# Kernel optimization log

Hardware: AMD Instinct MI355X
Metric: run time of the kernel (lower is better)

Reference implementation:

```python
import jax, jax.numpy as jnp
import numpy as np

QWEN_H = 2048
SNN_H = 512


def setup_inputs() -> dict:
    key = jax.random.key(0)
    k0, k1, k2, k3, k4 = jax.random.split(key, 5)
    hidden_states = jax.random.normal(k0, (4, 2048, QWEN_H), dtype=jnp.float32)
    # nn.Linear weights stored as [out, in]
    w_down = jax.random.normal(k1, (SNN_H, QWEN_H), dtype=jnp.float32) / np.sqrt(QWEN_H)
    w_up = jax.random.normal(k2, (QWEN_H, SNN_H), dtype=jnp.float32) / np.sqrt(SNN_H)
    w1 = jax.random.normal(k3, (SNN_H, SNN_H), dtype=jnp.float32) / np.sqrt(SNN_H)
    w2 = jax.random.normal(k4, (SNN_H, SNN_H), dtype=jnp.float32) / np.sqrt(SNN_H)
    residual_scale = jnp.float32(0.1)
    return {"hidden_states": hidden_states, "w_down": w_down, "w_up": w_up,
            "w1": w1, "w2": w2, "residual_scale": residual_scale}


def reference(hidden_states, w_down, w_up, w1, w2, residual_scale):
    # Faithful math of SNNMiddleLayer.forward. The spike pulse encode ->
    # SpikeFP32Linear (fp32 accumulation) -> pulse decode path is a lossless
    # FP32 spike encoding of an ordinary bias-free linear layer, so the
    # per-timestep loop computes exactly out_t = w2 @ (w1 @ proj_down(x_t)),
    # which we express as fused batched GEMMs over all timesteps.
    residual = hidden_states
    x = jnp.einsum('bsq,hq->bsh', hidden_states, w_down)   # proj_down
    h = jnp.einsum('bsh,oh->bso', x, w1)                   # snn_linear1
    o = jnp.einsum('bso,po->bsp', h, w2)                   # snn_linear2
    out = jnp.einsum('bsp,qp->bsq', o, w_up)               # proj_up
    return residual + residual_scale * out
```

## Files before the change

### kernel.cpp

```cpp
#include <hip/hip_runtime.h>
#include <hip/hip_bf16.h>
#include <stdint.h>

using bf16 = __hip_bfloat16;
typedef __attribute__((ext_vector_type(8))) short bf16x8;
typedef __attribute__((ext_vector_type(4))) float f32x4;

__device__ __forceinline__ void async_load16(const void* g, void* l) {
    __builtin_amdgcn_global_load_lds(
        (__attribute__((address_space(1))) const void*)g,
        (__attribute__((address_space(3))) void*)l,
        16, 0, 0);
}

__device__ __forceinline__ void cvt_block_2048(const float* __restrict__ src,
                                               bf16* __restrict__ dst, int relblk) {
    int i = (relblk * 256 + (int)threadIdx.x) * 8;
    float4 f0 = *(const float4*)(src + i);
    float4 f1 = *(const float4*)(src + i + 4);
    union { bf16 h[8]; uint4 u; } o;
    o.h[0] = __float2bfloat16(f0.x); o.h[1] = __float2bfloat16(f0.y);
    o.h[2] = __float2bfloat16(f0.z); o.h[3] = __float2bfloat16(f0.w);
    o.h[4] = __float2bfloat16(f1.x); o.h[5] = __float2bfloat16(f1.y);
    o.h[6] = __float2bfloat16(f1.z); o.h[7] = __float2bfloat16(f1.w);
    *(uint4*)(dst + i) = o.u;
}

__device__ __forceinline__ void transp_tile(const float* __restrict__ src,
                                            bf16* __restrict__ dst, int R, int C,
                                            int tile, int ntx, bf16 (*sh)[33]) {
    const int bx = (tile % ntx) * 32, by = (tile / ntx) * 32;
    const int lx = threadIdx.x & 31;
    const int ly4 = ((int)threadIdx.x >> 5) * 4;
#pragma unroll
    for (int r = 0; r < 4; ++r)
        sh[ly4 + r][lx] = __float2bfloat16(src[(size_t)(by + ly4 + r) * C + bx + lx]);
    __syncthreads();
#pragma unroll
    for (int r = 0; r < 4; ++r)
        dst[(size_t)(bx + ly4 + r) * R + by + lx] = sh[lx][ly4 + r];
}

__global__ __launch_bounds__(256) void prep(
    const float* __restrict__ hs, bf16* __restrict__ hsb,
    const float* __restrict__ w1, bf16* __restrict__ w1b,
    const float* __restrict__ wup, bf16* __restrict__ wub,
    const float* __restrict__ wd, bf16* __restrict__ wdt,
    const float* __restrict__ w2, bf16* __restrict__ w2t) {
    __shared__ bf16 sh[32][33];
    int b = blockIdx.x;
    if (b < 8192)       cvt_block_2048(hs, hsb, b);
    else if (b < 8320)  cvt_block_2048(w1, w1b, b - 8192);
    else if (b < 8832)  cvt_block_2048(wup, wub, b - 8320);
    else if (b < 9856)  transp_tile(wd, wdt, 512, 2048, b - 8832, 64, sh);
    else                transp_tile(w2, w2t, 512, 512, b - 9856, 16, sh);
}

template<int BN, int EPI>
__device__ __forceinline__ void gemm_core(
    const bf16* __restrict__ A, const bf16* __restrict__ B,
    bf16* __restrict__ Cb, float* __restrict__ Cf,
    const float* __restrict__ Res, const float* __restrict__ sp,
    int N, int K, int bxi, int byi, bf16* As, bf16* Bs)
{
    constexpr int BM = 128;
    constexpr int NJ = BN / 32;
    static_assert(BN == 64 || BN == 128, "BN");

    const int tid  = threadIdx.x;
    const int wave = tid >> 6;
    const int lane = tid & 63;
    const int wm = wave >> 1, wn = wave & 1;
    const size_t bm = (size_t)bxi * BM;
    const size_t bn = (size_t)byi * BN;

    f32x4 acc[4][NJ];
#pragma unroll
    for (int i = 0; i < 4; ++i)
#pragma unroll
        for (int j = 0; j < NJ; ++j)
            acc[i][j] = (f32x4){0.f, 0.f, 0.f, 0.f};

    const int srow  = lane >> 3;
    const int scol8 = (lane & 7) ^ srow;

    for (int k0 = 0; k0 < K; k0 += 64) {
        constexpr int TOT = (BM + BN) / 8;
#pragma unroll
        for (int c = 0; c < TOT / 4; ++c) {
            const int cc = wave + c * 4;
            if (cc < BM / 8) {
                const int rb = cc * 8;
                async_load16(A + (bm + rb + srow) * (size_t)K + k0 + scol8 * 8, &As[rb * 64]);
            } else {
                const int rb = (cc - BM / 8) * 8;
                async_load16(B + (bn + rb + srow) * (size_t)K + k0 + scol8 * 8, &Bs[rb * 64]);
            }
        }
        __syncthreads();

#pragma unroll
        for (int kk = 0; kk < 2; ++kk) {
            bf16x8 af[4], bfr[NJ];
#pragma unroll
            for (int i = 0; i < 4; ++i) {
                const int r  = wm * 64 + i * 16 + (lane & 15);
                const int c8 = kk * 4 + (lane >> 4);
                af[i] = *(const bf16x8*)&As[(size_t)(r * 8 + (c8 ^ (r & 7))) * 8];
            }
#pragma unroll
            for (int j = 0; j < NJ; ++j) {
                const int r  = wn * (BN / 2) + j * 16 + (lane & 15);
                const int c8 = kk * 4 + (lane >> 4);
                bfr[j] = *(const bf16x8*)&Bs[(size_t)(r * 8 + (c8 ^ (r & 7))) * 8];
            }
#pragma unroll
            for (int i = 0; i < 4; ++i)
#pragma unroll
                for (int j = 0; j < NJ; ++j)
                    acc[i][j] = __builtin_amdgcn_mfma_f32_16x16x32_bf16(af[i], bfr[j], acc[i][j], 0, 0, 0);
        }
        __syncthreads();
    }

    const int col_l = lane & 15;
    const int row_l = (lane >> 4) * 4;
    if (EPI == 0) {
#pragma unroll
        for (int i = 0; i < 4; ++i)
#pragma unroll
            for (int j = 0; j < NJ; ++j)
#pragma unroll
                for (int r = 0; r < 4; ++r) {
                    size_t row = bm + wm * 64 + i * 16 + row_l + r;
                    size_t col = bn + wn * (BN / 2) + j * 16 + col_l;
                    Cb[row * (size_t)N + col] = __float2bfloat16(acc[i][j][r]);
                }
    } else {
        const float s = *sp;
        float* lds_f = (float*)As + wave * (16 * 68);
#pragma unroll
        for (int i = 0; i < 4; ++i) {
#pragma unroll
            for (int j = 0; j < NJ; ++j)
#pragma unroll
                for (int r = 0; r < 4; ++r)
                    lds_f[(row_l + r) * 68 + j * 16 + col_l] = acc[i][j][r];
            __syncthreads();
#pragma unroll
            for (int rh = 0; rh < 2; ++rh)
#pragma unroll
                for (int ch = 0; ch < 2; ++ch) {
                    const int r16 = rh * 8 + (lane >> 3);
                    const int cb  = (lane & 7) * 4 + ch * 32;
                    float4 v = *(float4*)&lds_f[r16 * 68 + cb];
                    size_t row = bm + wm * 64 + i * 16 + r16;
                    size_t col = bn + wn * 64 + cb;
                    size_t idx = row * (size_t)N + col;
                    float4 rv = *(const float4*)&Res[idx];
                    float4 o;
                    o.x = rv.x + s * v.x; o.y = rv.y + s * v.y;
                    o.z = rv.z + s * v.z; o.w = rv.w + s * v.w;
                    *(float4*)&Cf[idx] = o;
                }
            __syncthreads();
        }
    }
}

template<int BN, int EPI>
__global__ __launch_bounds__(256) void gemm_bf16(
    const bf16* __restrict__ A, const bf16* __restrict__ B,
    bf16* __restrict__ Cb, float* __restrict__ Cf,
    const float* __restrict__ Res, const float* __restrict__ sp, int N, int K) {
    __shared__ __align__(16) bf16 smem[(128 + BN) * 64];
    gemm_core<BN, EPI>(A, B, Cb, Cf, Res, sp, N, K, blockIdx.y, blockIdx.x,
                       smem, smem + 128 * 64);
}

__global__ __launch_bounds__(256) void gemm_ru(
    const bf16* __restrict__ A0, const bf16* __restrict__ B0, bf16* __restrict__ C0,
    int N0, int K0, int nb0, int nt0,
    const bf16* __restrict__ A1, const bf16* __restrict__ B1, bf16* __restrict__ C1,
    int N1, int K1, int nt1) {
    __shared__ __align__(16) bf16 smem[(128 + 64) * 64];
    int b = blockIdx.x;
    if (b < nb0)
        gemm_core<64, 0>(A0, B0, C0, nullptr, nullptr, nullptr, N0, K0,
                         b / nt0, b % nt0, smem, smem + 128 * 64);
    else {
        b -= nb0;
        gemm_core<64, 0>(A1, B1, C1, nullptr, nullptr, nullptr, N1, K1,
                         b / nt1, b % nt1, smem, smem + 128 * 64);
    }
}

extern "C" void kernel_launch(void* const* d_in, const int* in_sizes, int n_in,
                              void* d_out, int out_size, void* d_ws, size_t ws_size,
                              hipStream_t stream) {
    const float* hs     = (const float*)d_in[0];
    const float* w_down = (const float*)d_in[1];
    const float* w_up   = (const float*)d_in[2];
    const float* w1     = (const float*)d_in[3];
    const float* w2     = (const float*)d_in[4];
    const float* rs     = (const float*)d_in[5];

    char* ws = (char*)d_ws;
    bf16* hs_b  = (bf16*)(ws + 0);
    bf16* x_b   = (bf16*)(ws + 33554432);
    bf16* w1_b  = (bf16*)(ws + 41943040);
    bf16* wu_b  = (bf16*)(ws + 42467328);
    bf16* wdt_b = (bf16*)(ws + 44564480);
    bf16* w2t_b = (bf16*)(ws + 46661632);
    bf16* Rm    = (bf16*)(ws + 47185920);
    bf16* Um    = (bf16*)(ws + 49283072);

    prep<<<dim3(10112), dim3(256), 0, stream>>>(hs, hs_b, w1, w1_b, w_up, wu_b,
                                                w_down, wdt_b, w2, w2t_b);
    gemm_ru<<<dim3(256), dim3(256), 0, stream>>>(w1_b, wdt_b, Rm, 2048, 512, 128, 32,
                                                 wu_b, w2t_b, Um, 512, 512, 8);
    gemm_bf16<64, 0><<<dim3(8, 64), dim3(256), 0, stream>>>(hs_b, Rm, x_b, nullptr,
                                                            nullptr, nullptr, 512, 2048);
    gemm_bf16<128, 1><<<dim3(16, 64), dim3(256), 0, stream>>>(x_b, Um, nullptr, (float*)d_out,
                                                              hs, rs, 2048, 512);
}
```

Before: 218.5 us.

## Overlap hidden-state conversion with weight GEMMs, double K-step, prefetch residual

Moves the large fp32-to-bf16 conversion of hidden_states out of the weight-prep kernel into the same launch as the small weight-product GEMMs. The bulk conversion then fills the GPU alongside those few blocks instead of serialising before them. The big down-projection GEMM now stages two 64-wide K slices per barrier, halving the number of synchronisations at the cost of doubled LDS. The final GEMM loads half of its residual tile into registers before the main loop so that global read overlaps the MFMA work, which raises register pressure.

```diff
diff --git a/kernel.cpp b/kernel.cpp
--- a/kernel.cpp
+++ b/kernel.cpp
@@ -26,37 +26,31 @@
     *(uint4*)(dst + i) = o.u;
 }
 
-__device__ __forceinline__ void transp_tile(const float* __restrict__ src,
-                                            bf16* __restrict__ dst, int R, int C,
-                                            int tile, int ntx, bf16 (*sh)[33]) {
-    const int bx = (tile % ntx) * 32, by = (tile / ntx) * 32;
-    const int lx = threadIdx.x & 31;
-    const int ly4 = ((int)threadIdx.x >> 5) * 4;
-#pragma unroll
-    for (int r = 0; r < 4; ++r)
-        sh[ly4 + r][lx] = __float2bfloat16(src[(size_t)(by + ly4 + r) * C + bx + lx]);
-    __syncthreads();
-#pragma unroll
-    for (int r = 0; r < 4; ++r)
-        dst[(size_t)(bx + ly4 + r) * R + by + lx] = sh[lx][ly4 + r];
-}
-
-__global__ __launch_bounds__(256) void prep(
-    const float* __restrict__ hs, bf16* __restrict__ hsb,
+__global__ __launch_bounds__(256) void prep_w(
     const float* __restrict__ w1, bf16* __restrict__ w1b,
     const float* __restrict__ wup, bf16* __restrict__ wub,
     const float* __restrict__ wd, bf16* __restrict__ wdt,
     const float* __restrict__ w2, bf16* __restrict__ w2t) {
     __shared__ bf16 sh[32][33];
     int b = blockIdx.x;
-    if (b < 8192)       cvt_block_2048(hs, hsb, b);
-    else if (b < 8320)  cvt_block_2048(w1, w1b, b - 8192);
-    else if (b < 8832)  cvt_block_2048(wup, wub, b - 8320);
-    else if (b < 9856)  transp_tile(wd, wdt, 512, 2048, b - 8832, 64, sh);
-    else                transp_tile(w2, w2t, 512, 512, b - 9856, 16, sh);
-}
-
-template<int BN, int EPI>
+    if (b < 128)       { cvt_block_2048(w1, w1b, b); return; }
+    if (b < 640)       { cvt_block_2048(wup, wub, b - 128); return; }
+    const float* src; bf16* dst; int R, C, tile, ntx;
+    if (b < 1664) { src = wd; dst = wdt; R = 512; C = 2048; tile = b - 640; ntx = 64; }
+    else          { src = w2; dst = w2t; R = 512; C = 512;  tile = b - 1664; ntx = 16; }
+    const int bx = (tile % ntx) * 32, by = (tile / ntx) * 32;
+    const int lx = threadIdx.x & 31;
+    const int ly4 = ((int)threadIdx.x >> 5) * 4;
+#pragma unroll
+    for (int r = 0; r < 4; ++r)
+        sh[ly4 + r][lx] = __float2bfloat16(src[(size_t)(by + ly4 + r) * C + bx + lx]);
+    __syncthreads();
+#pragma unroll
+    for (int r = 0; r < 4; ++r)
+        dst[(size_t)(bx + ly4 + r) * R + by + lx] = sh[lx][ly4 + r];
+}
+
+template<int BN, int EPI, int NP>
 __device__ __forceinline__ void gemm_core(
     const bf16* __restrict__ A, const bf16* __restrict__ B,
     bf16* __restrict__ Cb, float* __restrict__ Cf,
@@ -84,35 +78,56 @@
     const int srow  = lane >> 3;
     const int scol8 = (lane & 7) ^ srow;
 
-    for (int k0 = 0; k0 < K; k0 += 64) {
+    float4 res_pre[EPI ? 8 : 1];
+    if (EPI) {
+        const int r16 = lane >> 3;
+        const int cbb = (lane & 7) * 4;
+#pragma unroll
+        for (int i = 0; i < 2; ++i)
+#pragma unroll
+            for (int rh = 0; rh < 2; ++rh)
+#pragma unroll
+                for (int ch = 0; ch < 2; ++ch) {
+                    size_t row = bm + wm * 64 + i * 16 + rh * 8 + r16;
+                    size_t col = bn + wn * 64 + cbb + ch * 32;
+                    res_pre[i * 4 + rh * 2 + ch] = *(const float4*)&Res[row * (size_t)N + col];
+                }
+    }
+
+    for (int k0 = 0; k0 < K; k0 += 64 * NP) {
         constexpr int TOT = (BM + BN) / 8;
 #pragma unroll
-        for (int c = 0; c < TOT / 4; ++c) {
-            const int cc = wave + c * 4;
-            if (cc < BM / 8) {
-                const int rb = cc * 8;
-                async_load16(A + (bm + rb + srow) * (size_t)K + k0 + scol8 * 8, &As[rb * 64]);
-            } else {
-                const int rb = (cc - BM / 8) * 8;
-                async_load16(B + (bn + rb + srow) * (size_t)K + k0 + scol8 * 8, &Bs[rb * 64]);
+        for (int p = 0; p < NP; ++p)
+#pragma unroll
+            for (int c = 0; c < TOT / 4; ++c) {
+                const int cc = wave + c * 4;
+                if (cc < BM / 8) {
+                    const int rb = cc * 8;
+                    async_load16(A + (bm + rb + srow) * (size_t)K + k0 + p * 64 + scol8 * 8,
+                                 &As[p * BM * 64 + rb * 64]);
+                } else {
+                    const int rb = (cc - BM / 8) * 8;
+                    async_load16(B + (bn + rb + srow) * (size_t)K + k0 + p * 64 + scol8 * 8,
+                                 &Bs[p * BN * 64 + rb * 64]);
+                }
             }
-        }
         __syncthreads();
 
 #pragma unroll
-        for (int kk = 0; kk < 2; ++kk) {
+        for (int kk = 0; kk < 2 * NP; ++kk) {
+            const bf16* Ap = As + (kk >> 1) * BM * 64;
+            const bf16* Bp = Bs + (kk >> 1) * BN * 64;
+            const int c8 = (kk & 1) * 4 + (lane >> 4);
             bf16x8 af[4], bfr[NJ];
 #pragma unroll
             for (int i = 0; i < 4; ++i) {
-                const int r  = wm * 64 + i * 16 + (lane & 15);
-                const int c8 = kk * 4 + (lane >> 4);
-                af[i] = *(const bf16x8*)&As[(size_t)(r * 8 + (c8 ^ (r & 7))) * 8];
+                const int r = wm * 64 + i * 16 + (lane & 15);
+                af[i] = *(const bf16x8*)&Ap[(size_t)(r * 8 + (c8 ^ (r & 7))) * 8];
             }
 #pragma unroll
             for (int j = 0; j < NJ; ++j) {
-                const int r  = wn * (BN / 2) + j * 16 + (lane & 15);
-                const int c8 = kk * 4 + (lane >> 4);
-                bfr[j] = *(const bf16x8*)&Bs[(size_t)(r * 8 + (c8 ^ (r & 7))) * 8];
+                const int r = wn * (BN / 2) + j * 16 + (lane & 15);
+                bfr[j] = *(const bf16x8*)&Bp[(size_t)(r * 8 + (c8 ^ (r & 7))) * 8];
             }
 #pragma unroll
             for (int i = 0; i < 4; ++i)
@@ -157,7 +172,8 @@
                     size_t row = bm + wm * 64 + i * 16 + r16;
                     size_t col = bn + wn * 64 + cb;
                     size_t idx = row * (size_t)N + col;
-                    float4 rv = *(const float4*)&Res[idx];
+                    float4 rv = (i < 2) ? res_pre[i * 4 + rh * 2 + ch]
+                                        : *(const float4*)&Res[idx];
                     float4 o;
                     o.x = rv.x + s * v.x; o.y = rv.y + s * v.y;
                     o.z = rv.z + s * v.z; o.w = rv.w + s * v.w;
@@ -168,31 +184,31 @@
     }
 }
 
-template<int BN, int EPI>
+template<int BN, int EPI, int NP>
 __global__ __launch_bounds__(256) void gemm_bf16(
     const bf16* __restrict__ A, const bf16* __restrict__ B,
     bf16* __restrict__ Cb, float* __restrict__ Cf,
     const float* __restrict__ Res, const float* __restrict__ sp, int N, int K) {
-    __shared__ __align__(16) bf16 smem[(128 + BN) * 64];
-    gemm_core<BN, EPI>(A, B, Cb, Cf, Res, sp, N, K, blockIdx.y, blockIdx.x,
-                       smem, smem + 128 * 64);
-}
-
-__global__ __launch_bounds__(256) void gemm_ru(
+    __shared__ __align__(16) bf16 smem[(128 + BN) * 64 * NP];
+    gemm_core<BN, EPI, NP>(A, B, Cb, Cf, Res, sp, N, K, blockIdx.y, blockIdx.x,
+                           smem, smem + 128 * 64 * NP);
+}
+
+__global__ __launch_bounds__(256) void ru_cvt(
     const bf16* __restrict__ A0, const bf16* __restrict__ B0, bf16* __restrict__ C0,
-    int N0, int K0, int nb0, int nt0,
     const bf16* __restrict__ A1, const bf16* __restrict__ B1, bf16* __restrict__ C1,
-    int N1, int K1, int nt1) {
+    const float* __restrict__ hs, bf16* __restrict__ hsb) {
     __shared__ __align__(16) bf16 smem[(128 + 64) * 64];
     int b = blockIdx.x;
-    if (b < nb0)
-        gemm_core<64, 0>(A0, B0, C0, nullptr, nullptr, nullptr, N0, K0,
-                         b / nt0, b % nt0, smem, smem + 128 * 64);
-    else {
-        b -= nb0;
-        gemm_core<64, 0>(A1, B1, C1, nullptr, nullptr, nullptr, N1, K1,
-                         b / nt1, b % nt1, smem, smem + 128 * 64);
-    }
+    if (b < 128)
+        gemm_core<64, 0, 1>(A0, B0, C0, nullptr, nullptr, nullptr, 2048, 512,
+                            b / 32, b % 32, smem, smem + 128 * 64);
+    else if (b < 256) {
+        int bb = b - 128;
+        gemm_core<64, 0, 1>(A1, B1, C1, nullptr, nullptr, nullptr, 512, 512,
+                            bb / 8, bb % 8, smem, smem + 128 * 64);
+    } else
+        cvt_block_2048(hs, hsb, b - 256);
 }
 
 extern "C" void kernel_launch(void* const* d_in, const int* in_sizes, int n_in,
@@ -215,12 +231,10 @@
     bf16* Rm    = (bf16*)(ws + 47185920);
     bf16* Um    = (bf16*)(ws + 49283072);
 
-    prep<<<dim3(10112), dim3(256), 0, stream>>>(hs, hs_b, w1, w1_b, w_up, wu_b,
-                                                w_down, wdt_b, w2, w2t_b);
-    gemm_ru<<<dim3(256), dim3(256), 0, stream>>>(w1_b, wdt_b, Rm, 2048, 512, 128, 32,
-                                                 wu_b, w2t_b, Um, 512, 512, 8);
-    gemm_bf16<64, 0><<<dim3(8, 64), dim3(256), 0, stream>>>(hs_b, Rm, x_b, nullptr,
-                                                            nullptr, nullptr, 512, 2048);
-    gemm_bf16<128, 1><<<dim3(16, 64), dim3(256), 0, stream>>>(x_b, Um, nullptr, (float*)d_out,
-                                                              hs, rs, 2048, 512);
-}
+    prep_w<<<dim3(1920), dim3(256), 0, stream>>>(w1, w1_b, w_up, wu_b, w_down, wdt_b, w2, w2t_b);
+    ru_cvt<<<dim3(256 + 8192), dim3(256), 0, stream>>>(w1_b, wdt_b, Rm, wu_b, w2t_b, Um, hs, hs_b);
+    gemm_bf16<64, 0, 2><<<dim3(8, 64), dim3(256), 0, stream>>>(hs_b, Rm, x_b, nullptr,
+                                                               nullptr, nullptr, 512, 2048);
+    gemm_bf16<128, 1, 1><<<dim3(16, 64), dim3(256), 0, stream>>>(x_b, Um, nullptr, (float*)d_out,
+                                                                 hs, rs, 2048, 512);
+}
```

Result: faster. 211.6 us (-3.1%).
